# Optimization experiments

Measured on AMD Instinct MI355X. Metric: run time of the kernel, lower is better.

## Reference

```python
import jax, jax.numpy as jnp
import numpy as np

E, T, D_IN, D_H = 8, 2048, 2048, 5632


def setup_inputs() -> dict:
    key = jax.random.key(0)
    kx, kg, kd, ku = jax.random.split(key, 4)
    scale = 0.02  # init_std-like scaling for weights
    return {
        "x": jax.random.normal(kx, (E, T, D_IN), dtype=jnp.float32),
        "gate_proj": jax.random.normal(kg, (E, D_IN, D_H), dtype=jnp.float32) * scale,
        "down_proj": jax.random.normal(kd, (E, D_IN, D_H), dtype=jnp.float32) * scale,
        "up_proj": jax.random.normal(ku, (E, D_H, D_IN), dtype=jnp.float32) * scale,
        "tokens_per_expert": T,
    }


def reference(x, gate_proj, down_proj, up_proj, tokens_per_expert):
    # ep_size=1: dispatch/combine are identity. Grouped SwiGLU per expert.
    # x: [E, T, d_in]; gate/down: [E, d_in, d_h]; up: [E, d_h, d_in]
    g = jnp.einsum('etd,edh->eth', x, gate_proj)
    u = jnp.einsum('etd,edh->eth', x, down_proj)
    h = jax.nn.silu(g) * u  # [E, T, d_h]
    out = jnp.einsum('eth,ehd->etd', h, up_proj)  # [E, T, d_in]
    return out
```

## Files before the change

### kernel.cpp

```cpp
#include <hip/hip_runtime.h>
#include <hip/hip_bf16.h>


#define NEXP 8
#define TT   2048
#define DIN  2048
#define DH   5632

using short8 = __attribute__((ext_vector_type(8))) short;
using f32x4  = __attribute__((ext_vector_type(4))) float;

static __device__ __forceinline__ unsigned short f2bf(float f) {
    unsigned int i = __float_as_uint(f);
    return (unsigned short)((i + 0x7FFFu + ((i >> 16) & 1u)) >> 16);
}
static __device__ __forceinline__ void gld16(const void* g, void* l) {
    __builtin_amdgcn_global_load_lds(
        (const __attribute__((address_space(1))) void*)g,
        (__attribute__((address_space(3))) void*)l, 16, 0, 0);
}

__global__ __launch_bounds__(512, 2) void gemm_gu(
    const unsigned short* __restrict__ Xb,
    const unsigned short* __restrict__ Wgt,
    const unsigned short* __restrict__ Wdt,
    unsigned short* __restrict__ Hb)
{
    __shared__ __align__(16) unsigned short lds[65536];

    const int tid  = threadIdx.x;
    const int wave = tid >> 6, lane = tid & 63;
    const int l15 = lane & 15, l4 = lane >> 4;
    const int wr = wave >> 2, wc = wave & 3;

    const int orig = blockIdx.x;
    const int e    = orig & 7;
    const int w    = orig >> 3;
    const int r32  = w & 31;
    const int m0   = (r32 & 7) * 256;
    const int n0   = ((w >> 5) * 4 + (r32 >> 3)) * 128;

    const int K = DIN, NT = DIN >> 6;

    const unsigned short* Ae = Xb  + (size_t)e * TT * DIN;
    const unsigned short* Gp = Wgt + (size_t)e * DH * DIN + (size_t)n0 * K;
    const unsigned short* Dp = Wdt + (size_t)e * DH * DIN + (size_t)n0 * K;

    const int c0 = tid, c1 = 512 + tid;
    const int cs0 = c0 ^ ((c0 >> 3) & 7), cs1 = c1 ^ ((c1 >> 3) & 7);
    const int row0 = cs0 >> 3, col0 = (cs0 & 7) * 8;
    const int row1 = cs1 >> 3, col1 = (cs1 & 7) * 8;

    int ibA[4][2], ibB[2][2];
#pragma unroll
    for (int s = 0; s < 4; ++s)
#pragma unroll
        for (int ks = 0; ks < 2; ++ks) {
            const int r = wr * 64 + s * 16 + l15;
            ibA[s][ks] = (r * 128 + ks * 64 + l4 * 16) ^ ((r & 7) << 4);
        }
#pragma unroll
    for (int s = 0; s < 2; ++s)
#pragma unroll
        for (int ks = 0; ks < 2; ++ks) {
            const int r = wc * 32 + s * 16 + l15;
            ibB[s][ks] = (r * 128 + ks * 64 + l4 * 16) ^ ((r & 7) << 4);
        }

    f32x4 acc[8][4] = {};
    short8 Aq[4][2], Gq[2][2], Dq[2][2];

    auto stageA = [&](int ro, int kk, int slot) {
        gld16(Ae + (size_t)(m0 + ro + row0) * K + (kk + col0), &lds[slot * 8192 + wave * 512]);
        gld16(Ae + (size_t)(m0 + ro + row1) * K + (kk + col1), &lds[slot * 8192 + 4096 + wave * 512]);
    };
    auto stageW = [&](const unsigned short* p, int kk, int slot) {
        gld16(p + (size_t)row0 * K + (kk + col0), &lds[slot * 8192 + wave * 512]);
        gld16(p + (size_t)row1 * K + (kk + col1), &lds[slot * 8192 + 4096 + wave * 512]);
    };

    stageA(0, 0, 0);  stageW(Gp, 0, 1);  stageW(Dp, 0, 2);  stageA(128, 0, 3);
    stageA(0, 64, 4); stageW(Gp, 64, 5); stageW(Dp, 64, 6);
    asm volatile("s_waitcnt vmcnt(6)" ::: "memory");
    asm volatile("s_barrier" ::: "memory");

    const char* ldsc = (const char*)lds;
    for (int t = 0; t < NT; ++t) {
        const int sA0 = ((4 * t + 0) & 7) * 16384;
        const int sG  = ((4 * t + 1) & 7) * 16384;
        const int sD  = ((4 * t + 2) & 7) * 16384;
        const int sA1 = ((4 * t + 3) & 7) * 16384;

#pragma unroll
        for (int s = 0; s < 4; ++s) {
            Aq[s][0] = *(const short8*)(ldsc + sA0 + ibA[s][0]);
            Aq[s][1] = *(const short8*)(ldsc + sA0 + ibA[s][1]);
        }
#pragma unroll
        for (int s = 0; s < 2; ++s) {
            Gq[s][0] = *(const short8*)(ldsc + sG + ibB[s][0]);
            Gq[s][1] = *(const short8*)(ldsc + sG + ibB[s][1]);
        }
        if (t + 1 < NT) stageA(128, (t + 1) * 64, (4 * t + 7) & 7);
        asm volatile("s_barrier" ::: "memory");
        asm volatile("s_waitcnt lgkmcnt(0)" ::: "memory");
        __builtin_amdgcn_sched_barrier(0);
        __builtin_amdgcn_s_setprio(1);
#pragma unroll
        for (int m = 0; m < 4; ++m)
#pragma unroll
            for (int n = 0; n < 2; ++n) {
                acc[m][n] = __builtin_amdgcn_mfma_f32_16x16x32_bf16(Aq[m][0], Gq[n][0], acc[m][n], 0, 0, 0);
                acc[m][n] = __builtin_amdgcn_mfma_f32_16x16x32_bf16(Aq[m][1], Gq[n][1], acc[m][n], 0, 0, 0);
            }
        __builtin_amdgcn_s_setprio(0);
        asm volatile("s_barrier" ::: "memory");

#pragma unroll
        for (int s = 0; s < 2; ++s) {
            Dq[s][0] = *(const short8*)(ldsc + sD + ibB[s][0]);
            Dq[s][1] = *(const short8*)(ldsc + sD + ibB[s][1]);
        }
        if (t + 2 < NT) stageA(0, (t + 2) * 64, (4 * t + 8) & 7);
        asm volatile("s_barrier" ::: "memory");
        asm volatile("s_waitcnt lgkmcnt(0)" ::: "memory");
        __builtin_amdgcn_sched_barrier(0);
        __builtin_amdgcn_s_setprio(1);
#pragma unroll
        for (int m = 0; m < 4; ++m)
#pragma unroll
            for (int n = 0; n < 2; ++n) {
                acc[m][2 + n] = __builtin_amdgcn_mfma_f32_16x16x32_bf16(Aq[m][0], Dq[n][0], acc[m][2 + n], 0, 0, 0);
                acc[m][2 + n] = __builtin_amdgcn_mfma_f32_16x16x32_bf16(Aq[m][1], Dq[n][1], acc[m][2 + n], 0, 0, 0);
            }
        __builtin_amdgcn_s_setprio(0);
        asm volatile("s_barrier" ::: "memory");

#pragma unroll
        for (int s = 0; s < 4; ++s) {
            Aq[s][0] = *(const short8*)(ldsc + sA1 + ibA[s][0]);
            Aq[s][1] = *(const short8*)(ldsc + sA1 + ibA[s][1]);
        }
        if (t + 2 < NT) stageW(Gp, (t + 2) * 64, (4 * t + 9) & 7);
        asm volatile("s_barrier" ::: "memory");
        asm volatile("s_waitcnt lgkmcnt(0)" ::: "memory");
        __builtin_amdgcn_sched_barrier(0);
        __builtin_amdgcn_s_setprio(1);
#pragma unroll
        for (int m = 0; m < 4; ++m)
#pragma unroll
            for (int n = 0; n < 2; ++n) {
                acc[4 + m][2 + n] = __builtin_amdgcn_mfma_f32_16x16x32_bf16(Aq[m][0], Dq[n][0], acc[4 + m][2 + n], 0, 0, 0);
                acc[4 + m][2 + n] = __builtin_amdgcn_mfma_f32_16x16x32_bf16(Aq[m][1], Dq[n][1], acc[4 + m][2 + n], 0, 0, 0);
            }
        __builtin_amdgcn_s_setprio(0);
        asm volatile("s_barrier" ::: "memory");

        if (t + 2 < NT) stageW(Dp, (t + 2) * 64, (4 * t + 10) & 7);
        asm volatile("s_barrier" ::: "memory");
        __builtin_amdgcn_s_setprio(1);
#pragma unroll
        for (int m = 0; m < 4; ++m)
#pragma unroll
            for (int n = 0; n < 2; ++n) {
                acc[4 + m][n] = __builtin_amdgcn_mfma_f32_16x16x32_bf16(Aq[m][0], Gq[n][0], acc[4 + m][n], 0, 0, 0);
                acc[4 + m][n] = __builtin_amdgcn_mfma_f32_16x16x32_bf16(Aq[m][1], Gq[n][1], acc[4 + m][n], 0, 0, 0);
            }
        __builtin_amdgcn_s_setprio(0);
        if (t < NT - 2)       asm volatile("s_waitcnt vmcnt(6)" ::: "memory");
        else if (t == NT - 2) asm volatile("s_waitcnt vmcnt(0)" ::: "memory");
        asm volatile("s_barrier" ::: "memory");
    }

    unsigned short* He = Hb + (size_t)e * TT * DH;
#pragma unroll
    for (int fm = 0; fm < 8; ++fm) {
        const int row_b = m0 + (fm >> 2) * 128 + wr * 64 + (fm & 3) * 16 + l4 * 4;
#pragma unroll
        for (int nr = 0; nr < 2; ++nr) {
            const int col = n0 + wc * 32 + nr * 16 + l15;
#pragma unroll
            for (int j = 0; j < 4; ++j) {
                const float g = acc[fm][nr][j];
                const float u = acc[fm][2 + nr][j];
                const float h = g / (1.f + __expf(-g)) * u;
                He[(size_t)(row_b + j) * DH + col] = f2bf(h);
            }
        }
    }
}

__global__ __launch_bounds__(512, 2) void gemm_out(
    const unsigned short* __restrict__ Ab,
    const unsigned short* __restrict__ Btb,
    float* __restrict__ Cf)
{
    __shared__ __align__(16) unsigned short lds[65536];

    const int tid  = threadIdx.x;
    const int wave = tid >> 6, lane = tid & 63;
    const int l15 = lane & 15, l4 = lane >> 4;
    const int wr = wave >> 2, wc = wave & 3;

    const int orig = blockIdx.x;
    const int e    = orig & 7;
    const int w    = orig >> 3;
    const int r32  = w & 31;
    const int m0   = (r32 & 7) * 256;
    const int n0   = ((w >> 5) * 4 + (r32 >> 3)) * 256;

    const int M = TT, N = DIN, K = DH, NT = K >> 6;
    const unsigned short* Ae = Ab  + (size_t)e * TT * DH;
    const unsigned short* Be = Btb + (size_t)e * DIN * DH;

    const int c0 = tid, c1 = 512 + tid;
    const int cs0 = c0 ^ ((c0 >> 3) & 7), cs1 = c1 ^ ((c1 >> 3) & 7);
    const int row0 = cs0 >> 3, col0 = (cs0 & 7) * 8;
    const int row1 = cs1 >> 3, col1 = (cs1 & 7) * 8;

    int ibA[4][2], ibB[2][2];
#pragma unroll
    for (int s = 0; s < 4; ++s)
#pragma unroll
        for (int ks = 0; ks < 2; ++ks) {
            const int r = wr * 64 + s * 16 + l15;
            ibA[s][ks] = (r * 128 + ks * 64 + l4 * 16) ^ ((r & 7) << 4);
        }
#pragma unroll
    for (int s = 0; s < 2; ++s)
#pragma unroll
        for (int ks = 0; ks < 2; ++ks) {
            const int r = wc * 32 + s * 16 + l15;
            ibB[s][ks] = (r * 128 + ks * 64 + l4 * 16) ^ ((r & 7) << 4);
        }

    f32x4 acc[8][4] = {};
    short8 Aq[4][2], B0q[2][2], B1q[2][2];

    auto stageA = [&](int ro, int kk, int slot) {
        gld16(Ae + (size_t)(m0 + ro + row0) * K + (kk + col0), &lds[slot * 8192 + wave * 512]);
        gld16(Ae + (size_t)(m0 + ro + row1) * K + (kk + col1), &lds[slot * 8192 + 4096 + wave * 512]);
    };
    auto stageB = [&](int co, int kk, int slot) {
        gld16(Be + (size_t)(n0 + co + row0) * K + (kk + col0), &lds[slot * 8192 + wave * 512]);
        gld16(Be + (size_t)(n0 + co + row1) * K + (kk + col1), &lds[slot * 8192 + 4096 + wave * 512]);
    };

    stageA(0, 0, 0); stageB(0, 0, 1); stageB(128, 0, 2); stageA(128, 0, 3);
    stageA(0, 64, 4); stageB(0, 64, 5); stageB(128, 64, 6);
    asm volatile("s_waitcnt vmcnt(6)" ::: "memory");
    asm volatile("s_barrier" ::: "memory");

    const char* ldsc = (const char*)lds;
    for (int t = 0; t < NT; ++t) {
        const int sA0 = ((4 * t + 0) & 7) * 16384;
        const int sB0 = ((4 * t + 1) & 7) * 16384;
        const int sB1 = ((4 * t + 2) & 7) * 16384;
        const int sA1 = ((4 * t + 3) & 7) * 16384;

#pragma unroll
        for (int s = 0; s < 4; ++s) {
            Aq[s][0] = *(const short8*)(ldsc + sA0 + ibA[s][0]);
            Aq[s][1] = *(const short8*)(ldsc + sA0 + ibA[s][1]);
        }
#pragma unroll
        for (int s = 0; s < 2; ++s) {
            B0q[s][0] = *(const short8*)(ldsc + sB0 + ibB[s][0]);
            B0q[s][1] = *(const short8*)(ldsc + sB0 + ibB[s][1]);
        }
        if (t + 1 < NT) stageA(128, (t + 1) * 64, (4 * t + 7) & 7);
        asm volatile("s_barrier" ::: "memory");
        asm volatile("s_waitcnt lgkmcnt(0)" ::: "memory");
        __builtin_amdgcn_sched_barrier(0);
        __builtin_amdgcn_s_setprio(1);
#pragma unroll
        for (int m = 0; m < 4; ++m)
#pragma unroll
            for (int n = 0; n < 2; ++n) {
                acc[m][n] = __builtin_amdgcn_mfma_f32_16x16x32_bf16(Aq[m][0], B0q[n][0], acc[m][n], 0, 0, 0);
                acc[m][n] = __builtin_amdgcn_mfma_f32_16x16x32_bf16(Aq[m][1], B0q[n][1], acc[m][n], 0, 0, 0);
            }
        __builtin_amdgcn_s_setprio(0);
        asm volatile("s_barrier" ::: "memory");

#pragma unroll
        for (int s = 0; s < 2; ++s) {
            B1q[s][0] = *(const short8*)(ldsc + sB1 + ibB[s][0]);
            B1q[s][1] = *(const short8*)(ldsc + sB1 + ibB[s][1]);
        }
        if (t + 2 < NT) stageA(0, (t + 2) * 64, (4 * t + 8) & 7);
        asm volatile("s_barrier" ::: "memory");
        asm volatile("s_waitcnt lgkmcnt(0)" ::: "memory");
        __builtin_amdgcn_sched_barrier(0);
        __builtin_amdgcn_s_setprio(1);
#pragma unroll
        for (int m = 0; m < 4; ++m)
#pragma unroll
            for (int n = 0; n < 2; ++n) {
                acc[m][2 + n] = __builtin_amdgcn_mfma_f32_16x16x32_bf16(Aq[m][0], B1q[n][0], acc[m][2 + n], 0, 0, 0);
                acc[m][2 + n] = __builtin_amdgcn_mfma_f32_16x16x32_bf16(Aq[m][1], B1q[n][1], acc[m][2 + n], 0, 0, 0);
            }
        __builtin_amdgcn_s_setprio(0);
        asm volatile("s_barrier" ::: "memory");

#pragma unroll
        for (int s = 0; s < 4; ++s) {
            Aq[s][0] = *(const short8*)(ldsc + sA1 + ibA[s][0]);
            Aq[s][1] = *(const short8*)(ldsc + sA1 + ibA[s][1]);
        }
        if (t + 2 < NT) stageB(0, (t + 2) * 64, (4 * t + 9) & 7);
        asm volatile("s_barrier" ::: "memory");
        asm volatile("s_waitcnt lgkmcnt(0)" ::: "memory");
        __builtin_amdgcn_sched_barrier(0);
        __builtin_amdgcn_s_setprio(1);
#pragma unroll
        for (int m = 0; m < 4; ++m)
#pragma unroll
            for (int n = 0; n < 2; ++n) {
                acc[4 + m][2 + n] = __builtin_amdgcn_mfma_f32_16x16x32_bf16(Aq[m][0], B1q[n][0], acc[4 + m][2 + n], 0, 0, 0);
                acc[4 + m][2 + n] = __builtin_amdgcn_mfma_f32_16x16x32_bf16(Aq[m][1], B1q[n][1], acc[4 + m][2 + n], 0, 0, 0);
            }
        __builtin_amdgcn_s_setprio(0);
        asm volatile("s_barrier" ::: "memory");

        if (t + 2 < NT) stageB(128, (t + 2) * 64, (4 * t + 10) & 7);
        asm volatile("s_barrier" ::: "memory");
        __builtin_amdgcn_s_setprio(1);
#pragma unroll
        for (int m = 0; m < 4; ++m)
#pragma unroll
            for (int n = 0; n < 2; ++n) {
                acc[4 + m][n] = __builtin_amdgcn_mfma_f32_16x16x32_bf16(Aq[m][0], B0q[n][0], acc[4 + m][n], 0, 0, 0);
                acc[4 + m][n] = __builtin_amdgcn_mfma_f32_16x16x32_bf16(Aq[m][1], B0q[n][1], acc[4 + m][n], 0, 0, 0);
            }
        __builtin_amdgcn_s_setprio(0);
        if (t < NT - 2)       asm volatile("s_waitcnt vmcnt(6)" ::: "memory");
        else if (t == NT - 2) asm volatile("s_waitcnt vmcnt(0)" ::: "memory");
        asm volatile("s_barrier" ::: "memory");
    }

    float* Ce = Cf + (size_t)e * TT * DIN;
#pragma unroll
    for (int fm = 0; fm < 8; ++fm) {
        const int row_b = (fm >> 2) * 128 + wr * 64 + (fm & 3) * 16 + l4 * 4;
#pragma unroll
        for (int fn = 0; fn < 4; ++fn) {
            const int col = n0 + (fn >> 1) * 128 + wc * 32 + (fn & 1) * 16 + l15;
#pragma unroll
            for (int j = 0; j < 4; ++j)
                Ce[(size_t)(m0 + row_b + j) * N + col] = acc[fm][fn][j];
        }
    }
}

__global__ __launch_bounds__(256) void transpose2_f32_bf16(
    const float* __restrict__ in0, const float* __restrict__ in1,
    unsigned short* __restrict__ out, int R, int C, size_t ies, size_t oes)
{
    const int z = blockIdx.z;
    const float* in = ((z < NEXP) ? in0 : in1) + (size_t)(z & 7) * ies;
    out += (size_t)z * oes;
    __shared__ unsigned short t[64][65];
    const int tid = threadIdx.x;
    const int lr = tid >> 4, lc = (tid & 15) * 4;
    const int r0 = blockIdx.y * 64, c0 = blockIdx.x * 64;
#pragma unroll
    for (int i = 0; i < 4; ++i) {
        const int row = lr + i * 16;
        const float4 v = *(const float4*)(in + (size_t)(r0 + row) * C + c0 + lc);
        t[row][lc + 0] = f2bf(v.x); t[row][lc + 1] = f2bf(v.y);
        t[row][lc + 2] = f2bf(v.z); t[row][lc + 3] = f2bf(v.w);
    }
    __syncthreads();
#pragma unroll
    for (int i = 0; i < 4; ++i) {
        const int crow = lr + i * 16;
        ushort4 wv;
        wv.x = t[lc + 0][crow]; wv.y = t[lc + 1][crow];
        wv.z = t[lc + 2][crow]; wv.w = t[lc + 3][crow];
        *(ushort4*)(out + (size_t)(c0 + crow) * R + r0 + lc) = wv;
    }
}

__global__ __launch_bounds__(256) void conv_f32_bf16(
    const float* __restrict__ in, unsigned short* __restrict__ out, int n4)
{
    int i = blockIdx.x * 256 + threadIdx.x;
    const int stride = gridDim.x * 256;
    for (; i < n4; i += stride) {
        const float4 v = ((const float4*)in)[i];
        ushort4 wv;
        wv.x = f2bf(v.x); wv.y = f2bf(v.y); wv.z = f2bf(v.z); wv.w = f2bf(v.w);
        ((ushort4*)out)[i] = wv;
    }
}

extern "C" void kernel_launch(void* const* d_in, const int* in_sizes, int n_in,
                              void* d_out, int out_size, void* d_ws, size_t ws_size,
                              hipStream_t stream)
{
    const float* x  = (const float*)d_in[0];
    const float* wg = (const float*)d_in[1];
    const float* wd = (const float*)d_in[2];
    const float* wu = (const float*)d_in[3];
    float* out = (float*)d_out;

    const size_t XSZ = (size_t)TT * DIN;
    const size_t WSZ = (size_t)DIN * DH;
    unsigned short* xb  = (unsigned short*)d_ws;
    unsigned short* wgt = xb  + (size_t)NEXP * XSZ;
    unsigned short* wdt = wgt + (size_t)NEXP * WSZ;
    unsigned short* hb  = wdt + (size_t)NEXP * WSZ;

    conv_f32_bf16<<<4096, 256, 0, stream>>>(x, xb, (int)(NEXP * XSZ / 4));
    transpose2_f32_bf16<<<dim3(DH / 64, DIN / 64, NEXP * 2), 256, 0, stream>>>(
        wg, wd, wgt, DIN, DH, WSZ, WSZ);
    gemm_gu<<<NEXP * (TT / 256) * (DH / 128), 512, 0, stream>>>(xb, wgt, wdt, hb);
    transpose2_f32_bf16<<<dim3(DIN / 64, DH / 64, NEXP), 256, 0, stream>>>(
        wu, wu, wgt, DH, DIN, WSZ, WSZ);
    gemm_out<<<NEXP * (TT / 256) * (DIN / 256), 512, 0, stream>>>(hb, wgt, out);
}
```

Before: 1.258 ms.

## Retile gate/up GEMM to 128x128 tiles with 4 waves and 5-slot LDS ring

Restructures the fused gate/up GEMM from 512-thread blocks with 256-row tiles to 256-thread blocks computing a 128x128 output tile, where each wave owns a 64x64 region for both gate and up. The LDS pipeline becomes a 5-slot rotating buffer with fewer barriers per K step and different vmcnt waits. The launch grid doubles to match the smaller tiles. This aims to cut barrier overhead and raise occupancy and per-wave MFMA density, but it reuses each weight tile across fewer rows of X, which adds global traffic.

```diff
diff --git a/kernel.cpp b/kernel.cpp
--- a/kernel.cpp
+++ b/kernel.cpp
@@ -20,169 +20,172 @@
         (__attribute__((address_space(3))) void*)l, 16, 0, 0);
 }
 
-__global__ __launch_bounds__(512, 2) void gemm_gu(
+__global__ __launch_bounds__(256, 2) void gemm_gu(
     const unsigned short* __restrict__ Xb,
     const unsigned short* __restrict__ Wgt,
     const unsigned short* __restrict__ Wdt,
     unsigned short* __restrict__ Hb)
 {
-    __shared__ __align__(16) unsigned short lds[65536];
+    __shared__ __align__(16) unsigned short lds[40960];
 
     const int tid  = threadIdx.x;
     const int wave = tid >> 6, lane = tid & 63;
     const int l15 = lane & 15, l4 = lane >> 4;
-    const int wr = wave >> 2, wc = wave & 3;
-
-    const int orig = blockIdx.x;
-    const int e    = orig & 7;
-    const int w    = orig >> 3;
-    const int r32  = w & 31;
-    const int m0   = (r32 & 7) * 256;
-    const int n0   = ((w >> 5) * 4 + (r32 >> 3)) * 128;
+    const int wr = wave >> 1, wc = wave & 1;
+
+    const int bid = blockIdx.x;
+    const int e   = bid & 7;
+    const int w   = bid >> 3;
+    const int m0  = (w & 15) * 128;
+    const int n0  = (w >> 4) * 128;
 
     const int K = DIN, NT = DIN >> 6;
 
-    const unsigned short* Ae = Xb  + (size_t)e * TT * DIN;
+    const unsigned short* Ae = Xb  + (size_t)e * TT * DIN + (size_t)m0 * K;
     const unsigned short* Gp = Wgt + (size_t)e * DH * DIN + (size_t)n0 * K;
     const unsigned short* Dp = Wdt + (size_t)e * DH * DIN + (size_t)n0 * K;
-
-    const int c0 = tid, c1 = 512 + tid;
-    const int cs0 = c0 ^ ((c0 >> 3) & 7), cs1 = c1 ^ ((c1 >> 3) & 7);
-    const int row0 = cs0 >> 3, col0 = (cs0 & 7) * 8;
-    const int row1 = cs1 >> 3, col1 = (cs1 & 7) * 8;
-
-    int ibA[4][2], ibB[2][2];
+    unsigned short* He = Hb + (size_t)e * TT * DH;
+
+    size_t loff[4];
+    int dofs[4];
+#pragma unroll
+    for (int k = 0; k < 4; ++k) {
+        const int c = k * 256 + tid;
+        const int cs = c ^ ((c >> 3) & 7);
+        loff[k] = (size_t)(cs >> 3) * K + (cs & 7) * 8;
+        dofs[k] = k * 4096 + wave * 1024;
+    }
+
+    int ibA[4][2], ibB[4][2];
 #pragma unroll
     for (int s = 0; s < 4; ++s)
 #pragma unroll
         for (int ks = 0; ks < 2; ++ks) {
-            const int r = wr * 64 + s * 16 + l15;
-            ibA[s][ks] = (r * 128 + ks * 64 + l4 * 16) ^ ((r & 7) << 4);
-        }
-#pragma unroll
-    for (int s = 0; s < 2; ++s)
-#pragma unroll
-        for (int ks = 0; ks < 2; ++ks) {
-            const int r = wc * 32 + s * 16 + l15;
-            ibB[s][ks] = (r * 128 + ks * 64 + l4 * 16) ^ ((r & 7) << 4);
-        }
-
-    f32x4 acc[8][4] = {};
-    short8 Aq[4][2], Gq[2][2], Dq[2][2];
-
-    auto stageA = [&](int ro, int kk, int slot) {
-        gld16(Ae + (size_t)(m0 + ro + row0) * K + (kk + col0), &lds[slot * 8192 + wave * 512]);
-        gld16(Ae + (size_t)(m0 + ro + row1) * K + (kk + col1), &lds[slot * 8192 + 4096 + wave * 512]);
+            const int rA = wr * 64 + s * 16 + l15;
+            ibA[s][ks] = (rA * 128 + ks * 64 + l4 * 16) ^ ((rA & 7) << 4);
+            const int rB = wc * 64 + s * 16 + l15;
+            ibB[s][ks] = (rB * 128 + ks * 64 + l4 * 16) ^ ((rB & 7) << 4);
+        }
+
+    f32x4 accG[4][4] = {}, accU[4][4] = {};
+    short8 Aq[4][2], Bq[2][2];
+
+    char* ldsb = (char*)lds;
+    const char* ldsc = (const char*)lds;
+    auto stageU = [&](const unsigned short* p, int kk, int slot) {
+#pragma unroll
+        for (int k = 0; k < 4; ++k)
+            gld16(p + kk + loff[k], ldsb + slot * 16384 + dofs[k]);
     };
-    auto stageW = [&](const unsigned short* p, int kk, int slot) {
-        gld16(p + (size_t)row0 * K + (kk + col0), &lds[slot * 8192 + wave * 512]);
-        gld16(p + (size_t)row1 * K + (kk + col1), &lds[slot * 8192 + 4096 + wave * 512]);
-    };
-
-    stageA(0, 0, 0);  stageW(Gp, 0, 1);  stageW(Dp, 0, 2);  stageA(128, 0, 3);
-    stageA(0, 64, 4); stageW(Gp, 64, 5); stageW(Dp, 64, 6);
-    asm volatile("s_waitcnt vmcnt(6)" ::: "memory");
+    auto w5 = [](int x) { return x >= 5 ? x - 5 : x; };
+
+    stageU(Ae, 0, 0); stageU(Gp, 0, 1); stageU(Dp, 0, 2);
+    asm volatile("s_waitcnt vmcnt(0)" ::: "memory");
     asm volatile("s_barrier" ::: "memory");
 
-    const char* ldsc = (const char*)lds;
+    int q = 0;
     for (int t = 0; t < NT; ++t) {
-        const int sA0 = ((4 * t + 0) & 7) * 16384;
-        const int sG  = ((4 * t + 1) & 7) * 16384;
-        const int sD  = ((4 * t + 2) & 7) * 16384;
-        const int sA1 = ((4 * t + 3) & 7) * 16384;
+        const int bA = q * 16384;
+        const int bG = w5(q + 1) * 16384;
+        const int bD = w5(q + 2) * 16384;
+        const int stA = w5(q + 3);
+        const int stG = w5(q + 4);
 
 #pragma unroll
         for (int s = 0; s < 4; ++s) {
-            Aq[s][0] = *(const short8*)(ldsc + sA0 + ibA[s][0]);
-            Aq[s][1] = *(const short8*)(ldsc + sA0 + ibA[s][1]);
-        }
-#pragma unroll
-        for (int s = 0; s < 2; ++s) {
-            Gq[s][0] = *(const short8*)(ldsc + sG + ibB[s][0]);
-            Gq[s][1] = *(const short8*)(ldsc + sG + ibB[s][1]);
-        }
-        if (t + 1 < NT) stageA(128, (t + 1) * 64, (4 * t + 7) & 7);
-        asm volatile("s_barrier" ::: "memory");
-        asm volatile("s_waitcnt lgkmcnt(0)" ::: "memory");
-        __builtin_amdgcn_sched_barrier(0);
-        __builtin_amdgcn_s_setprio(1);
-#pragma unroll
-        for (int m = 0; m < 4; ++m)
-#pragma unroll
-            for (int n = 0; n < 2; ++n) {
-                acc[m][n] = __builtin_amdgcn_mfma_f32_16x16x32_bf16(Aq[m][0], Gq[n][0], acc[m][n], 0, 0, 0);
-                acc[m][n] = __builtin_amdgcn_mfma_f32_16x16x32_bf16(Aq[m][1], Gq[n][1], acc[m][n], 0, 0, 0);
-            }
-        __builtin_amdgcn_s_setprio(0);
-        asm volatile("s_barrier" ::: "memory");
-
-#pragma unroll
-        for (int s = 0; s < 2; ++s) {
-            Dq[s][0] = *(const short8*)(ldsc + sD + ibB[s][0]);
-            Dq[s][1] = *(const short8*)(ldsc + sD + ibB[s][1]);
-        }
-        if (t + 2 < NT) stageA(0, (t + 2) * 64, (4 * t + 8) & 7);
-        asm volatile("s_barrier" ::: "memory");
-        asm volatile("s_waitcnt lgkmcnt(0)" ::: "memory");
-        __builtin_amdgcn_sched_barrier(0);
-        __builtin_amdgcn_s_setprio(1);
-#pragma unroll
-        for (int m = 0; m < 4; ++m)
-#pragma unroll
-            for (int n = 0; n < 2; ++n) {
-                acc[m][2 + n] = __builtin_amdgcn_mfma_f32_16x16x32_bf16(Aq[m][0], Dq[n][0], acc[m][2 + n], 0, 0, 0);
-                acc[m][2 + n] = __builtin_amdgcn_mfma_f32_16x16x32_bf16(Aq[m][1], Dq[n][1], acc[m][2 + n], 0, 0, 0);
-            }
-        __builtin_amdgcn_s_setprio(0);
-        asm volatile("s_barrier" ::: "memory");
-
-#pragma unroll
-        for (int s = 0; s < 4; ++s) {
-            Aq[s][0] = *(const short8*)(ldsc + sA1 + ibA[s][0]);
-            Aq[s][1] = *(const short8*)(ldsc + sA1 + ibA[s][1]);
-        }
-        if (t + 2 < NT) stageW(Gp, (t + 2) * 64, (4 * t + 9) & 7);
-        asm volatile("s_barrier" ::: "memory");
-        asm volatile("s_waitcnt lgkmcnt(0)" ::: "memory");
-        __builtin_amdgcn_sched_barrier(0);
-        __builtin_amdgcn_s_setprio(1);
-#pragma unroll
-        for (int m = 0; m < 4; ++m)
-#pragma unroll
-            for (int n = 0; n < 2; ++n) {
-                acc[4 + m][2 + n] = __builtin_amdgcn_mfma_f32_16x16x32_bf16(Aq[m][0], Dq[n][0], acc[4 + m][2 + n], 0, 0, 0);
-                acc[4 + m][2 + n] = __builtin_amdgcn_mfma_f32_16x16x32_bf16(Aq[m][1], Dq[n][1], acc[4 + m][2 + n], 0, 0, 0);
-            }
-        __builtin_amdgcn_s_setprio(0);
-        asm volatile("s_barrier" ::: "memory");
-
-        if (t + 2 < NT) stageW(Dp, (t + 2) * 64, (4 * t + 10) & 7);
-        asm volatile("s_barrier" ::: "memory");
-        __builtin_amdgcn_s_setprio(1);
-#pragma unroll
-        for (int m = 0; m < 4; ++m)
-#pragma unroll
-            for (int n = 0; n < 2; ++n) {
-                acc[4 + m][n] = __builtin_amdgcn_mfma_f32_16x16x32_bf16(Aq[m][0], Gq[n][0], acc[4 + m][n], 0, 0, 0);
-                acc[4 + m][n] = __builtin_amdgcn_mfma_f32_16x16x32_bf16(Aq[m][1], Gq[n][1], acc[4 + m][n], 0, 0, 0);
-            }
-        __builtin_amdgcn_s_setprio(0);
-        if (t < NT - 2)       asm volatile("s_waitcnt vmcnt(6)" ::: "memory");
+            Aq[s][0] = *(const short8*)(ldsc + bA + ibA[s][0]);
+            Aq[s][1] = *(const short8*)(ldsc + bA + ibA[s][1]);
+        }
+#pragma unroll
+        for (int s = 0; s < 2; ++s) {
+            Bq[s][0] = *(const short8*)(ldsc + bG + ibB[s][0]);
+            Bq[s][1] = *(const short8*)(ldsc + bG + ibB[s][1]);
+        }
+        if (t + 1 < NT) {
+            stageU(Ae, (t + 1) * 64, stA);
+            stageU(Gp, (t + 1) * 64, stG);
+        }
+        asm volatile("s_waitcnt lgkmcnt(0)" ::: "memory");
+        __builtin_amdgcn_sched_barrier(0);
+        __builtin_amdgcn_s_setprio(1);
+#pragma unroll
+        for (int m = 0; m < 4; ++m)
+#pragma unroll
+            for (int n = 0; n < 2; ++n) {
+                accG[m][n] = __builtin_amdgcn_mfma_f32_16x16x32_bf16(Aq[m][0], Bq[n][0], accG[m][n], 0, 0, 0);
+                accG[m][n] = __builtin_amdgcn_mfma_f32_16x16x32_bf16(Aq[m][1], Bq[n][1], accG[m][n], 0, 0, 0);
+            }
+        __builtin_amdgcn_s_setprio(0);
+        asm volatile("s_waitcnt vmcnt(8)" ::: "memory");
+        asm volatile("s_barrier" ::: "memory");
+        if (t + 1 < NT) stageU(Dp, (t + 1) * 64, q);
+
+#pragma unroll
+        for (int s = 0; s < 2; ++s) {
+            Bq[s][0] = *(const short8*)(ldsc + bG + ibB[2 + s][0]);
+            Bq[s][1] = *(const short8*)(ldsc + bG + ibB[2 + s][1]);
+        }
+        asm volatile("s_waitcnt lgkmcnt(0)" ::: "memory");
+        __builtin_amdgcn_sched_barrier(0);
+        __builtin_amdgcn_s_setprio(1);
+#pragma unroll
+        for (int m = 0; m < 4; ++m)
+#pragma unroll
+            for (int n = 0; n < 2; ++n) {
+                accG[m][2 + n] = __builtin_amdgcn_mfma_f32_16x16x32_bf16(Aq[m][0], Bq[n][0], accG[m][2 + n], 0, 0, 0);
+                accG[m][2 + n] = __builtin_amdgcn_mfma_f32_16x16x32_bf16(Aq[m][1], Bq[n][1], accG[m][2 + n], 0, 0, 0);
+            }
+        __builtin_amdgcn_s_setprio(0);
+
+#pragma unroll
+        for (int s = 0; s < 2; ++s) {
+            Bq[s][0] = *(const short8*)(ldsc + bD + ibB[s][0]);
+            Bq[s][1] = *(const short8*)(ldsc + bD + ibB[s][1]);
+        }
+        asm volatile("s_waitcnt lgkmcnt(0)" ::: "memory");
+        __builtin_amdgcn_sched_barrier(0);
+        __builtin_amdgcn_s_setprio(1);
+#pragma unroll
+        for (int m = 0; m < 4; ++m)
+#pragma unroll
+            for (int n = 0; n < 2; ++n) {
+                accU[m][n] = __builtin_amdgcn_mfma_f32_16x16x32_bf16(Aq[m][0], Bq[n][0], accU[m][n], 0, 0, 0);
+                accU[m][n] = __builtin_amdgcn_mfma_f32_16x16x32_bf16(Aq[m][1], Bq[n][1], accU[m][n], 0, 0, 0);
+            }
+        __builtin_amdgcn_s_setprio(0);
+
+#pragma unroll
+        for (int s = 0; s < 2; ++s) {
+            Bq[s][0] = *(const short8*)(ldsc + bD + ibB[2 + s][0]);
+            Bq[s][1] = *(const short8*)(ldsc + bD + ibB[2 + s][1]);
+        }
+        asm volatile("s_waitcnt lgkmcnt(0)" ::: "memory");
+        __builtin_amdgcn_sched_barrier(0);
+        __builtin_amdgcn_s_setprio(1);
+#pragma unroll
+        for (int m = 0; m < 4; ++m)
+#pragma unroll
+            for (int n = 0; n < 2; ++n) {
+                accU[m][2 + n] = __builtin_amdgcn_mfma_f32_16x16x32_bf16(Aq[m][0], Bq[n][0], accU[m][2 + n], 0, 0, 0);
+                accU[m][2 + n] = __builtin_amdgcn_mfma_f32_16x16x32_bf16(Aq[m][1], Bq[n][1], accU[m][2 + n], 0, 0, 0);
+            }
+        __builtin_amdgcn_s_setprio(0);
+        if (t < NT - 2)       asm volatile("s_waitcnt vmcnt(4)" ::: "memory");
         else if (t == NT - 2) asm volatile("s_waitcnt vmcnt(0)" ::: "memory");
         asm volatile("s_barrier" ::: "memory");
-    }
-
-    unsigned short* He = Hb + (size_t)e * TT * DH;
-#pragma unroll
-    for (int fm = 0; fm < 8; ++fm) {
-        const int row_b = m0 + (fm >> 2) * 128 + wr * 64 + (fm & 3) * 16 + l4 * 4;
-#pragma unroll
-        for (int nr = 0; nr < 2; ++nr) {
-            const int col = n0 + wc * 32 + nr * 16 + l15;
+        q = w5(q + 3);
+    }
+
+#pragma unroll
+    for (int m = 0; m < 4; ++m) {
+        const int row_b = m0 + wr * 64 + m * 16 + l4 * 4;
+#pragma unroll
+        for (int n = 0; n < 4; ++n) {
+            const int col = n0 + wc * 64 + n * 16 + l15;
 #pragma unroll
             for (int j = 0; j < 4; ++j) {
-                const float g = acc[fm][nr][j];
-                const float u = acc[fm][2 + nr][j];
+                const float g = accG[m][n][j];
+                const float u = accU[m][n][j];
                 const float h = g / (1.f + __expf(-g)) * u;
                 He[(size_t)(row_b + j) * DH + col] = f2bf(h);
             }
@@ -209,7 +212,7 @@
     const int m0   = (r32 & 7) * 256;
     const int n0   = ((w >> 5) * 4 + (r32 >> 3)) * 256;
 
-    const int M = TT, N = DIN, K = DH, NT = K >> 6;
+    const int N = DIN, K = DH, NT = K >> 6;
     const unsigned short* Ae = Ab  + (size_t)e * TT * DH;
     const unsigned short* Be = Btb + (size_t)e * DIN * DH;
 
@@ -415,7 +418,7 @@
     conv_f32_bf16<<<4096, 256, 0, stream>>>(x, xb, (int)(NEXP * XSZ / 4));
     transpose2_f32_bf16<<<dim3(DH / 64, DIN / 64, NEXP * 2), 256, 0, stream>>>(
         wg, wd, wgt, DIN, DH, WSZ, WSZ);
-    gemm_gu<<<NEXP * (TT / 256) * (DH / 128), 512, 0, stream>>>(xb, wgt, wdt, hb);
+    gemm_gu<<<NEXP * (TT / 128) * (DH / 128), 256, 0, stream>>>(xb, wgt, wdt, hb);
     transpose2_f32_bf16<<<dim3(DIN / 64, DH / 64, NEXP), 256, 0, stream>>>(
         wu, wu, wgt, DH, DIN, WSZ, WSZ);
     gemm_out<<<NEXP * (TT / 256) * (DIN / 256), 512, 0, stream>>>(hb, wgt, out);
```

After: 1.294 ms. 2.9% more time.
